# Performance work log

Measured on AMD Instinct MI355X. Metric: run time of the kernel, lower is better.

## Reference

```python
import jax, jax.numpy as jnp
import numpy as np

B, T, D = 4, 1024, 1024
H, DH = 8, 128           # heads, dim_head = dim // heads
E, FF = 8, 2048          # num_experts, expert hidden_dim
LN_EPS = 1e-5


def setup_inputs() -> dict:
    key = jax.random.key(0)
    ks = jax.random.split(key, 20)
    s = 0.02
    inp = {
        'v': jax.random.normal(ks[0], (B, T, D), jnp.float32),
        'k': jax.random.normal(ks[1], (B, T, D), jnp.float32),
        'q': jax.random.normal(ks[2], (B, T, D), jnp.float32),
        'noise': jax.random.normal(ks[3], (B * T, E), jnp.float32),
        # LayerNorm params (norm_v, norm_k, norm_q, norm_moe, moe output norm)
        'g_v': jnp.ones((D,)), 'b_v': jnp.zeros((D,)),
        'g_k': jnp.ones((D,)), 'b_k': jnp.zeros((D,)),
        'g_q': jnp.ones((D,)), 'b_q': jnp.zeros((D,)),
        'g_moe': jnp.ones((D,)), 'b_moe': jnp.zeros((D,)),
        'g_out': jnp.ones((D,)), 'b_out': jnp.zeros((D,)),
        # LinearAttention projections (q/k/v have no bias, out_proj has bias)
        'Wq': jax.random.normal(ks[4], (D, H * DH), jnp.float32) * s,
        'Wk': jax.random.normal(ks[5], (D, H * DH), jnp.float32) * s,
        'Wv': jax.random.normal(ks[6], (D, H * DH), jnp.float32) * s,
        'Wo': jax.random.normal(ks[7], (H * DH, D), jnp.float32) * s,
        'bo': jnp.zeros((D,)),
        # Router
        'Wr': jax.random.normal(ks[8], (D, E), jnp.float32) * s,
        'br': jnp.zeros((E,)),
        # Experts (stacked): dim -> FF -> dim
        'W1': jax.random.normal(ks[9], (E, D, FF), jnp.float32) * s,
        'b1': jnp.zeros((E, FF)),
        'W2': jax.random.normal(ks[10], (E, FF, D), jnp.float32) * s,
        'b2': jnp.zeros((E, D)),
        'top_k': 2,
    }
    return inp


def _ln(x, g, b):
    mu = x.mean(-1, keepdims=True)
    x0 = x - mu
    var = (x0 * x0).mean(-1, keepdims=True)
    return x0 * jax.lax.rsqrt(var + LN_EPS) * g + b


def reference(v, k, q, noise, g_v, b_v, g_k, b_k, g_q, b_q, g_moe, b_moe,
              g_out, b_out, Wq, Wk, Wv, Wo, bo, Wr, br, W1, b1, W2, b2, top_k):
    # --- LinearAttention over pre-normed v,k,q ---
    qh = jnp.einsum('btd,de->bte', _ln(q, g_q, b_q), Wq).reshape(B, T, H, DH)
    kh = jnp.einsum('btd,de->bte', _ln(k, g_k, b_k), Wk).reshape(B, T, H, DH)
    vh = jnp.einsum('btd,de->bte', _ln(v, g_v, b_v), Wv).reshape(B, T, H, DH)
    qf = jax.nn.elu(qh) + 1.0
    kf = jax.nn.elu(kh) + 1.0
    kv = jnp.einsum('bthd,bthe->bhde', kf, vh)          # [B,H,DH,DH]
    out = jnp.einsum('bthd,bhde->bthe', qf, kv)         # [B,T,H,DH]
    k_sum = kf.sum(axis=1) + 1e-6                       # [B,H,DH]
    denom = jnp.einsum('bthd,bhd->bth', qf, k_sum)[..., None]
    out = out / denom
    attn_out = jnp.einsum('bte,ed->btd', out.reshape(B, T, H * DH), Wo) + bo

    q_res = q + attn_out

    # --- MoEBlock: noisy top-k routing + expert MLPs + residual + LayerNorm ---
    x = _ln(q_res, g_moe, b_moe)
    xf = x.reshape(B * T, D)
    logits = xf @ Wr + br + noise * 0.1                 # noisy gating (randn/10)
    scores = jax.nn.softmax(logits, axis=-1)
    topk_s, topk_i = jax.lax.top_k(scores, top_k)       # [N,K]
    combine = (jax.nn.one_hot(topk_i, E, dtype=scores.dtype) * topk_s[..., None]).sum(1)  # [N,E]
    h = jax.nn.gelu(jnp.einsum('nd,edh->enh', xf, W1) + b1[:, None, :], approximate=False)
    eo = jnp.einsum('enh,ehd->end', h, W2) + b2[:, None, :]
    moe = jnp.einsum('end,ne->nd', eo, combine)         # weighted combine == masked dispatch
    moe_out = _ln(moe.reshape(B, T, D) + x, g_out, b_out)

    return q_res + moe_out
```

## Files before the change

### kernel.cpp

```cpp
#include <hip/hip_runtime.h>
#include <math.h>

typedef __attribute__((ext_vector_type(8))) short short8;
typedef __attribute__((ext_vector_type(4))) float f32x4;

#define LN_EPS 1e-5f

__device__ __forceinline__ float bf2f(unsigned short u) {
  unsigned int x = ((unsigned int)u) << 16;
  float f;
  __builtin_memcpy(&f, &x, 4);
  return f;
}
__device__ __forceinline__ unsigned short f2bf(float f) {
  unsigned int x;
  __builtin_memcpy(&x, &f, 4);
  x += 0x7fffu + ((x >> 16) & 1u);
  return (unsigned short)(x >> 16);
}

__device__ __forceinline__ void gload16(const void* g, void* l) {
  __builtin_amdgcn_global_load_lds(
      (__attribute__((address_space(1))) void*)(void*)g,
      (__attribute__((address_space(3))) void*)l, 16, 0, 0);
}

__device__ __forceinline__ void blockReduce2(float& a, float& b, float* s8) {
#pragma unroll
  for (int off = 32; off > 0; off >>= 1) {
    a += __shfl_down(a, off);
    b += __shfl_down(b, off);
  }
  const int w = threadIdx.x >> 6;
  if ((threadIdx.x & 63) == 0) { s8[w] = a; s8[4 + w] = b; }
  __syncthreads();
  a = s8[0] + s8[1] + s8[2] + s8[3];
  b = s8[4] + s8[5] + s8[6] + s8[7];
}

__global__ __launch_bounds__(256) void ln3_kernel(
    const float* __restrict__ q, const float* __restrict__ k, const float* __restrict__ v,
    const float* __restrict__ gq, const float* __restrict__ bq,
    const float* __restrict__ gk, const float* __restrict__ bk,
    const float* __restrict__ gv, const float* __restrict__ bv,
    unsigned short* __restrict__ oq, unsigned short* __restrict__ ok,
    unsigned short* __restrict__ ov) {
  __shared__ float s8[8];
  const int row = blockIdx.x, which = blockIdx.y;
  const float* x = which == 0 ? q : which == 1 ? k : v;
  const float* g = which == 0 ? gq : which == 1 ? gk : gv;
  const float* b = which == 0 ? bq : which == 1 ? bk : bv;
  unsigned short* o = which == 0 ? oq : which == 1 ? ok : ov;
  const float4 xv = ((const float4*)(x + (size_t)row * 1024))[threadIdx.x];
  float s = xv.x + xv.y + xv.z + xv.w;
  float s2 = xv.x * xv.x + xv.y * xv.y + xv.z * xv.z + xv.w * xv.w;
  blockReduce2(s, s2, s8);
  const float mu = s * (1.f / 1024.f);
  const float rs = rsqrtf(s2 * (1.f / 1024.f) - mu * mu + LN_EPS);
  const int c = threadIdx.x * 4;
  const float y[4] = {xv.x, xv.y, xv.z, xv.w};
#pragma unroll
  for (int j = 0; j < 4; ++j)
    o[(size_t)row * 1024 + c + j] = f2bf((y[j] - mu) * rs * g[c + j] + b[c + j]);
}

__global__ __launch_bounds__(256) void ln_moe_router_kernel(
    const float* __restrict__ qres, const float* __restrict__ g, const float* __restrict__ b,
    const float* __restrict__ Wr, const float* __restrict__ br,
    const float* __restrict__ noise,
    float* __restrict__ xf, unsigned short* __restrict__ xb,
    int* __restrict__ pick, float* __restrict__ pw) {
  __shared__ float s8[8];
  __shared__ float sacc[32];
  const int row = blockIdx.x;
  const float4 xv = ((const float4*)(qres + (size_t)row * 1024))[threadIdx.x];
  float s = xv.x + xv.y + xv.z + xv.w;
  float s2 = xv.x * xv.x + xv.y * xv.y + xv.z * xv.z + xv.w * xv.w;
  blockReduce2(s, s2, s8);
  const float mu = s * (1.f / 1024.f);
  const float rs = rsqrtf(s2 * (1.f / 1024.f) - mu * mu + LN_EPS);
  const int c = threadIdx.x * 4;
  const float yin[4] = {xv.x, xv.y, xv.z, xv.w};
  float y[4];
#pragma unroll
  for (int j = 0; j < 4; ++j) {
    y[j] = (yin[j] - mu) * rs * g[c + j] + b[c + j];
    xf[(size_t)row * 1024 + c + j] = y[j];
    xb[(size_t)row * 1024 + c + j] = f2bf(y[j]);
  }
  float acc[8] = {};
  const float4* wrv = (const float4*)(Wr + (size_t)c * 8);
#pragma unroll
  for (int j = 0; j < 4; ++j) {
    const float4 w0 = wrv[j * 2], w1 = wrv[j * 2 + 1];
    acc[0] += y[j] * w0.x; acc[1] += y[j] * w0.y;
    acc[2] += y[j] * w0.z; acc[3] += y[j] * w0.w;
    acc[4] += y[j] * w1.x; acc[5] += y[j] * w1.y;
    acc[6] += y[j] * w1.z; acc[7] += y[j] * w1.w;
  }
#pragma unroll
  for (int off = 32; off > 0; off >>= 1)
#pragma unroll
    for (int e = 0; e < 8; ++e) acc[e] += __shfl_down(acc[e], off);
  const int w = threadIdx.x >> 6;
  if ((threadIdx.x & 63) == 0)
#pragma unroll
    for (int e = 0; e < 8; ++e) sacc[w * 8 + e] = acc[e];
  __syncthreads();
  if (threadIdx.x == 0) {
    float lg[8], mx = -1e30f;
#pragma unroll
    for (int e = 0; e < 8; ++e) {
      lg[e] = sacc[e] + sacc[8 + e] + sacc[16 + e] + sacc[24 + e] + br[e] +
              0.1f * noise[(size_t)row * 8 + e];
      mx = fmaxf(mx, lg[e]);
    }
    float ssum = 0.f;
#pragma unroll
    for (int e = 0; e < 8; ++e) { lg[e] = expf(lg[e] - mx); ssum += lg[e]; }
    const float inv = 1.f / ssum;
#pragma unroll
    for (int e = 0; e < 8; ++e) lg[e] *= inv;
    int i1 = -1, i2 = -1;
    float m1 = -1.f, m2 = -1.f;
#pragma unroll
    for (int e = 0; e < 8; ++e) {
      if (lg[e] > m1) { m2 = m1; i2 = i1; m1 = lg[e]; i1 = e; }
      else if (lg[e] > m2) { m2 = lg[e]; i2 = e; }
    }
    pick[row * 2] = i1; pick[row * 2 + 1] = i2;
    pw[row * 2] = m1;  pw[row * 2 + 1] = m2;
  }
}

__global__ __launch_bounds__(1024) void route_build_kernel(
    const int* __restrict__ pick, const float* __restrict__ pw,
    int* __restrict__ seg, int* __restrict__ tok, float* __restrict__ wgt,
    int* __restrict__ slt) {
  __shared__ int cnt[8];
  __shared__ int segs[9];
  __shared__ int cur[8];
  const int tid = threadIdx.x;
  if (tid < 8) { cnt[tid] = 0; cur[tid] = 0; }
  __syncthreads();
  for (int i = tid; i < 8192; i += 1024) atomicAdd(&cnt[pick[i]], 1);
  __syncthreads();
  if (tid == 0) {
    int o = 0;
    for (int e = 0; e < 8; ++e) { segs[e] = o; o += (cnt[e] + 127) & ~127; }
    segs[8] = o;
  }
  __syncthreads();
  for (int i = tid; i < 9216; i += 1024) tok[i] = -1;
  if (tid < 9) seg[tid] = segs[tid];
  __syncthreads();
  for (int i = tid; i < 8192; i += 1024) {
    const int n = i >> 1, sl = i & 1;
    const int e = pick[i];
    const int p = atomicAdd(&cur[e], 1);
    const int gr = segs[e] + p;
    tok[gr] = n;
    wgt[gr] = pw[i];
    slt[gr] = sl;
  }
}

__global__ __launch_bounds__(256) void final_kernel(
    const float* __restrict__ eoS, const float* __restrict__ xf,
    const float* __restrict__ qres, const float* __restrict__ g,
    const float* __restrict__ b, float* __restrict__ out) {
  __shared__ float s8[8];
  const int row = blockIdx.x;
  const size_t SLOT = (size_t)4096 * 1024;
  const float4 m0 = ((const float4*)(eoS + (size_t)row * 1024))[threadIdx.x];
  const float4 m1 = ((const float4*)(eoS + SLOT + (size_t)row * 1024))[threadIdx.x];
  const float4 xv = ((const float4*)(xf + (size_t)row * 1024))[threadIdx.x];
  float y[4] = {m0.x + m1.x + xv.x, m0.y + m1.y + xv.y, m0.z + m1.z + xv.z,
                m0.w + m1.w + xv.w};
  float s = y[0] + y[1] + y[2] + y[3];
  float s2 = y[0] * y[0] + y[1] * y[1] + y[2] * y[2] + y[3] * y[3];
  blockReduce2(s, s2, s8);
  const float mu = s * (1.f / 1024.f);
  const float rs = rsqrtf(s2 * (1.f / 1024.f) - mu * mu + LN_EPS);
  const int c = threadIdx.x * 4;
#pragma unroll
  for (int j = 0; j < 4; ++j) {
    const size_t idx = (size_t)row * 1024 + c + j;
    out[idx] = qres[idx] + (y[j] - mu) * rs * g[c + j] + b[c + j];
  }
}

__global__ __launch_bounds__(256) void transposeB_kernel(
    const float* const* __restrict__ ins, unsigned short* const* __restrict__ outs,
    int R, int C) {
  __shared__ float t[32][33];
  const float* inz = ins[blockIdx.z];
  unsigned short* outz = outs[blockIdx.z];
  const int bx = blockIdx.x, by = blockIdx.y;
  const int tx = threadIdx.x & 31, ty = threadIdx.x >> 5;
#pragma unroll
  for (int i = 0; i < 32; i += 8)
    t[ty + i][tx] = inz[(size_t)(by * 32 + ty + i) * C + bx * 32 + tx];
  __syncthreads();
#pragma unroll
  for (int i = 0; i < 32; i += 8)
    outz[(size_t)(bx * 32 + ty + i) * R + by * 32 + tx] = f2bf(t[tx][ty + i]);
}

__global__ __launch_bounds__(256) void transpose8_kernel(
    const float* __restrict__ in, unsigned short* __restrict__ out, int R, int C) {
  __shared__ float t[32][33];
  const float* inz = in + (size_t)blockIdx.z * R * C;
  unsigned short* outz = out + (size_t)blockIdx.z * R * C;
  const int bx = blockIdx.x, by = blockIdx.y;
  const int tx = threadIdx.x & 31, ty = threadIdx.x >> 5;
#pragma unroll
  for (int i = 0; i < 32; i += 8)
    t[ty + i][tx] = inz[(size_t)(by * 32 + ty + i) * C + bx * 32 + tx];
  __syncthreads();
#pragma unroll
  for (int i = 0; i < 32; i += 8)
    outz[(size_t)(bx * 32 + ty + i) * R + by * 32 + tx] = f2bf(t[tx][ty + i]);
}

#define GEMM_BODY(GA0, GA1, GB, KDIM)                                              \
  f32x4 acc[4][4] = {};                                                            \
  for (int k0 = 0; k0 < (KDIM); k0 += 32) {                                        \
    gload16((GA0) + k0, lA);                                                       \
    gload16((GA1) + k0, lA + 16 * 32);                                             \
    gload16((GB) + k0, lB);                                                        \
    gload16((GB) + (size_t)16 * (KDIM) + k0, lB + 16 * 32);                        \
    __syncthreads();                                                               \
    short8 af[4], bfr[4];                                                          \
    const int arow = wr * 64 + (lane & 15);                                        \
    const int brow = wc * 64 + (lane & 15);                                        \
    const int kk = (lane >> 4) * 8;                                                \
    _Pragma("unroll") for (int m = 0; m < 4; ++m)                                  \
        af[m] = *(const short8*)&As[(arow + m * 16) * 32 + kk];                    \
    _Pragma("unroll") for (int n = 0; n < 4; ++n)                                  \
        bfr[n] = *(const short8*)&Bs[(brow + n * 16) * 32 + kk];                   \
    _Pragma("unroll") for (int m = 0; m < 4; ++m)                                  \
        _Pragma("unroll") for (int n = 0; n < 4; ++n)                              \
            acc[m][n] =                                                            \
                __builtin_amdgcn_mfma_f32_16x16x32_bf16(af[m], bfr[n], acc[m][n],  \
                                                        0, 0, 0);                  \
    __syncthreads();                                                               \
  }

__global__ __launch_bounds__(256) void gemm_qkv(
    const unsigned short* __restrict__ lnq, const unsigned short* __restrict__ lnk,
    const unsigned short* __restrict__ lnv, const unsigned short* __restrict__ WqT,
    const unsigned short* __restrict__ WkT, const unsigned short* __restrict__ WvT,
    unsigned short* __restrict__ qf, unsigned short* __restrict__ kf,
    unsigned short* __restrict__ vh) {
  __shared__ __align__(16) unsigned short As[128 * 32];
  __shared__ __align__(16) unsigned short Bs[128 * 32];
  const int z = blockIdx.z;
  const unsigned short* A = z == 0 ? lnq : z == 1 ? lnk : lnv;
  const unsigned short* Bt = z == 0 ? WqT : z == 1 ? WkT : WvT;
  unsigned short* outb = z == 0 ? qf : z == 1 ? kf : vh;
  const int K = 1024, N = 1024;
  const int tid = threadIdx.x;
  const int lane = tid & 63, w = tid >> 6;
  const int wr = w >> 1, wc = w & 1;
  const int row0 = blockIdx.y * 128, col0 = blockIdx.x * 128;
  const int sr = lane >> 2, sc = (lane & 3) * 8;
  const unsigned short* gA = A + (size_t)(row0 + w * 32 + sr) * K + sc;
  const unsigned short* gB = Bt + (size_t)(col0 + w * 32 + sr) * K + sc;
  unsigned short* lA = &As[(w * 32) * 32];
  unsigned short* lB = &Bs[(w * 32) * 32];
  GEMM_BODY(gA, gA + (size_t)16 * K, gB, K)
#pragma unroll
  for (int m = 0; m < 4; ++m) {
    const int rbase = row0 + wr * 64 + m * 16 + (lane >> 4) * 4;
#pragma unroll
    for (int n = 0; n < 4; ++n) {
      const int c = col0 + wc * 64 + n * 16 + (lane & 15);
#pragma unroll
      for (int r = 0; r < 4; ++r) {
        float v = acc[m][n][r];
        if (z < 2) v = v > 0.f ? v + 1.f : __expf(v);
        outb[(size_t)(rbase + r) * N + c] = f2bf(v);
      }
    }
  }
}

__global__ __launch_bounds__(256) void gemm_wo(
    const unsigned short* __restrict__ A, const unsigned short* __restrict__ Bt,
    float* __restrict__ outf, const float* __restrict__ bias,
    const float* __restrict__ addm) {
  __shared__ __align__(16) unsigned short As[128 * 32];
  __shared__ __align__(16) unsigned short Bs[128 * 32];
  const int K = 1024, N = 1024;
  const int tid = threadIdx.x;
  const int lane = tid & 63, w = tid >> 6;
  const int wr = w >> 1, wc = w & 1;
  const int row0 = blockIdx.y * 128, col0 = blockIdx.x * 128;
  const int sr = lane >> 2, sc = (lane & 3) * 8;
  const unsigned short* gA = A + (size_t)(row0 + w * 32 + sr) * K + sc;
  const unsigned short* gB = Bt + (size_t)(col0 + w * 32 + sr) * K + sc;
  unsigned short* lA = &As[(w * 32) * 32];
  unsigned short* lB = &Bs[(w * 32) * 32];
  GEMM_BODY(gA, gA + (size_t)16 * K, gB, K)
#pragma unroll
  for (int m = 0; m < 4; ++m) {
    const int rbase = row0 + wr * 64 + m * 16 + (lane >> 4) * 4;
#pragma unroll
    for (int n = 0; n < 4; ++n) {
      const int c = col0 + wc * 64 + n * 16 + (lane & 15);
#pragma unroll
      for (int r = 0; r < 4; ++r) {
        const size_t idx = (size_t)(rbase + r) * N + c;
        outf[idx] = acc[m][n][r] + bias[c] + addm[idx];
      }
    }
  }
}

template <int PHASE>
__global__ __launch_bounds__(256) void gemm_moe(
    const unsigned short* __restrict__ Asrc, const unsigned short* __restrict__ Ball,
    const float* __restrict__ bias_all, int K, int N,
    const int* __restrict__ seg, const int* __restrict__ tok,
    const float* __restrict__ wgt, const int* __restrict__ slt,
    unsigned short* __restrict__ Hb, float* __restrict__ eoS) {
  __shared__ __align__(16) unsigned short As[128 * 32];
  __shared__ __align__(16) unsigned short Bs[128 * 32];
  const int row0 = blockIdx.y * 128;
  if (row0 >= seg[8]) return;
  int e = 0;
  while (e < 7 && row0 >= seg[e + 1]) ++e;
  const int col0 = blockIdx.x * 128;
  const int tid = threadIdx.x;
  const int lane = tid & 63, w = tid >> 6;
  const int wr = w >> 1, wc = w & 1;
  const int sr = lane >> 2, sc = (lane & 3) * 8;
  const unsigned short* Bt = Ball + (size_t)e * N * K;

  const int gr0 = row0 + w * 32 + sr;
  const int gr1 = gr0 + 16;
  const unsigned short* gA0;
  const unsigned short* gA1;
  if constexpr (PHASE == 1) {
    const int t0 = tok[gr0], t1 = tok[gr1];
    gA0 = Asrc + (size_t)(t0 < 0 ? 0 : t0) * K + sc;
    gA1 = Asrc + (size_t)(t1 < 0 ? 0 : t1) * K + sc;
  } else {
    gA0 = Asrc + (size_t)gr0 * K + sc;
    gA1 = Asrc + (size_t)gr1 * K + sc;
  }
  const unsigned short* gB = Bt + (size_t)(col0 + w * 32 + sr) * K + sc;
  unsigned short* lA = &As[(w * 32) * 32];
  unsigned short* lB = &Bs[(w * 32) * 32];
  GEMM_BODY(gA0, gA1, gB, K)
#pragma unroll
  for (int m = 0; m < 4; ++m) {
    const int rloc = wr * 64 + m * 16 + (lane >> 4) * 4;
#pragma unroll
    for (int n = 0; n < 4; ++n) {
      const int c = col0 + wc * 64 + n * 16 + (lane & 15);
#pragma unroll
      for (int r = 0; r < 4; ++r) {
        const int gr = row0 + rloc + r;
        float v = acc[m][n][r] + bias_all[(size_t)e * N + c];
        if constexpr (PHASE == 1) {
          v = 0.5f * v * (1.f + erff(v * 0.70710678118654752f));
          Hb[(size_t)gr * N + c] = f2bf(v);
        } else {
          const int t = tok[gr];
          if (t >= 0)
            eoS[(size_t)slt[gr] * (4096 * 1024) + (size_t)t * N + c] = wgt[gr] * v;
        }
      }
    }
  }
}

__global__ __launch_bounds__(256) void kvpart_kernel(
    const unsigned short* __restrict__ kf, const unsigned short* __restrict__ vh,
    float* __restrict__ kvp, float* __restrict__ ksp) {
  const int bh = blockIdx.x;
  const int b = bh >> 3, h = bh & 7;
  const int ch = blockIdx.y;
  const int tid = threadIdx.x;
  const int d0 = (tid >> 4) * 8, e0 = (tid & 15) * 8;
  __shared__ unsigned short kb[64][128];
  __shared__ unsigned short vb[64][128];
  for (int i = tid; i < 1024; i += 256) {
    const int tt = i >> 4, dd = (i & 15) * 8;
    const size_t base = ((size_t)((b * 1024 + ch * 64 + tt) * 8 + h)) * 128 + dd;
    *(short8*)&kb[tt][dd] = *(const short8*)&kf[base];
    *(short8*)&vb[tt][dd] = *(const short8*)&vh[base];
  }
  __syncthreads();
  float acc[8][8] = {};
  float ks[8] = {};
  for (int tt = 0; tt < 64; ++tt) {
    float kv8[8], vv8[8];
    const short8 kr = *(const short8*)&kb[tt][d0];
    const short8 vr = *(const short8*)&vb[tt][e0];
#pragma unroll
    for (int j = 0; j < 8; ++j) {
      kv8[j] = bf2f((unsigned short)kr[j]);
      vv8[j] = bf2f((unsigned short)vr[j]);
    }
#pragma unroll
    for (int i = 0; i < 8; ++i)
#pragma unroll
      for (int j = 0; j < 8; ++j) acc[i][j] += kv8[i] * vv8[j];
    if ((tid & 15) == 0)
#pragma unroll
      for (int i = 0; i < 8; ++i) ks[i] += kv8[i];
  }
  const size_t obase = ((size_t)(ch * 32 + bh) * 128) * 128;
#pragma unroll
  for (int i = 0; i < 8; ++i)
#pragma unroll
    for (int j = 0; j < 8; ++j)
      kvp[obase + (size_t)(d0 + i) * 128 + e0 + j] = acc[i][j];
  if ((tid & 15) == 0)
#pragma unroll
    for (int i = 0; i < 8; ++i) ksp[(size_t)(ch * 32 + bh) * 128 + d0 + i] = ks[i];
}

__global__ __launch_bounds__(256) void kvreduce_kernel(
    const float* __restrict__ kvp, const float* __restrict__ ksp,
    unsigned short* __restrict__ kvb, float* __restrict__ ksum) {
  const int idx = blockIdx.x * 256 + threadIdx.x;
  const int CS = 32 * 128 * 128;
  float s = 0.f;
#pragma unroll
  for (int c = 0; c < 16; ++c) s += kvp[(size_t)c * CS + idx];
  kvb[idx] = f2bf(s);
  if (idx < 32 * 128) {
    float t = 1e-6f;
#pragma unroll
    for (int c = 0; c < 16; ++c) t += ksp[c * 4096 + idx];
    ksum[idx] = t;
  }
}

__global__ __launch_bounds__(256) void attnout_kernel(
    const unsigned short* __restrict__ qf, const unsigned short* __restrict__ kvb,
    const float* __restrict__ ksum, unsigned short* __restrict__ ctx) {
  const int bh = blockIdx.x, b = bh >> 3, h = bh & 7;
  const int tb = blockIdx.y;
  const int tid = threadIdx.x;
  __shared__ unsigned short kvl[128 * 128];
  __shared__ float ksl[128];
  __shared__ float denom[128];
  __shared__ unsigned short qfl[128 * 32];
  for (int i = tid; i < 16384; i += 256) kvl[i] = kvb[(size_t)bh * 16384 + i];
  if (tid < 128) ksl[tid] = ksum[bh * 128 + tid];
  __syncthreads();
  if (tid < 128) {
    const int t = tb * 128 + tid;
    const size_t qbase = ((size_t)((b * 1024 + t) * 8 + h)) * 128;
    float s = 0.f;
    for (int d = 0; d < 128; ++d) s += bf2f(qf[qbase + d]) * ksl[d];
    denom[tid] = s;
  }
  float acc[8][8] = {};
  const int t0 = (tid >> 4) * 8, e0 = (tid & 15) * 8;
  for (int dc = 0; dc < 128; dc += 32) {
    __syncthreads();
    for (int i = tid; i < 128 * 32; i += 256) {
      const int tt = i >> 5, dd = i & 31;
      qfl[i] = qf[((size_t)((b * 1024 + tb * 128 + tt) * 8 + h)) * 128 + dc + dd];
    }
    __syncthreads();
    for (int dd = 0; dd < 32; ++dd) {
      float kvrow[8];
#pragma unroll
      for (int j = 0; j < 8; ++j) kvrow[j] = bf2f(kvl[(dc + dd) * 128 + e0 + j]);
#pragma unroll
      for (int i = 0; i < 8; ++i) {
        const float qv = bf2f(qfl[(t0 + i) * 32 + dd]);
#pragma unroll
        for (int j = 0; j < 8; ++j) acc[i][j] += qv * kvrow[j];
      }
    }
  }
  __syncthreads();
#pragma unroll
  for (int i = 0; i < 8; ++i) {
    const int t = tb * 128 + t0 + i;
    const float inv = 1.f / denom[t0 + i];
#pragma unroll
    for (int j = 0; j < 8; ++j)
      ctx[((size_t)(b * 1024 + t)) * 1024 + h * 128 + e0 + j] = f2bf(acc[i][j] * inv);
  }
}

__global__ void setptr_kernel(const float* Wq, const float* Wk, const float* Wv,
                              const float* Wo, unsigned short* WqT, unsigned short* WkT,
                              unsigned short* WvT, unsigned short* WoT,
                              const float** ins, unsigned short** outs) {
  if (threadIdx.x == 0) {
    ins[0] = Wq; ins[1] = Wk; ins[2] = Wv; ins[3] = Wo;
    outs[0] = WqT; outs[1] = WkT; outs[2] = WvT; outs[3] = WoT;
  }
}

extern "C" void kernel_launch(void* const* d_in, const int* in_sizes, int n_in,
                              void* d_out, int out_size, void* d_ws, size_t ws_size,
                              hipStream_t stream) {
  (void)in_sizes; (void)n_in; (void)out_size; (void)ws_size;
  const float* vin  = (const float*)d_in[0];
  const float* kin  = (const float*)d_in[1];
  const float* qin  = (const float*)d_in[2];
  const float* noise = (const float*)d_in[3];
  const float* g_v = (const float*)d_in[4];  const float* b_v = (const float*)d_in[5];
  const float* g_k = (const float*)d_in[6];  const float* b_k = (const float*)d_in[7];
  const float* g_q = (const float*)d_in[8];  const float* b_q = (const float*)d_in[9];
  const float* g_moe = (const float*)d_in[10]; const float* b_moe = (const float*)d_in[11];
  const float* g_out = (const float*)d_in[12]; const float* b_out = (const float*)d_in[13];
  const float* Wq = (const float*)d_in[14];
  const float* Wk = (const float*)d_in[15];
  const float* Wv = (const float*)d_in[16];
  const float* Wo = (const float*)d_in[17];
  const float* bo = (const float*)d_in[18];
  const float* Wr = (const float*)d_in[19];
  const float* br = (const float*)d_in[20];
  const float* W1 = (const float*)d_in[21];
  const float* b1 = (const float*)d_in[22];
  const float* W2 = (const float*)d_in[23];
  const float* b2 = (const float*)d_in[24];
  float* out = (float*)d_out;

  const int NT = 4096, D = 1024, FF = 2048;
  const int MAXR = 9216;

  char* p = (char*)d_ws;
  auto alloc = [&](size_t bytes) {
    void* r = (void*)p;
    p += (bytes + 255) & ~(size_t)255;
    return r;
  };
  char* base0 = p;
  unsigned short* lnq = (unsigned short*)alloc((size_t)NT * D * 2);
  unsigned short* lnk = (unsigned short*)alloc((size_t)NT * D * 2);
  unsigned short* lnv = (unsigned short*)alloc((size_t)NT * D * 2);
  unsigned short* WqT = (unsigned short*)alloc((size_t)D * D * 2);
  unsigned short* WkT = (unsigned short*)alloc((size_t)D * D * 2);
  unsigned short* WvT = (unsigned short*)alloc((size_t)D * D * 2);
  unsigned short* WoT = (unsigned short*)alloc((size_t)D * D * 2);
  unsigned short* qf  = (unsigned short*)alloc((size_t)NT * D * 2);
  unsigned short* kf  = (unsigned short*)alloc((size_t)NT * D * 2);
  unsigned short* vh  = (unsigned short*)alloc((size_t)NT * D * 2);
  unsigned short* kvb = (unsigned short*)alloc((size_t)32 * 128 * 128 * 2);
  float* ksp  = (float*)alloc((size_t)16 * 32 * 128 * 4);
  float* ksum = (float*)alloc((size_t)32 * 128 * 4);
  unsigned short* ctx = (unsigned short*)alloc((size_t)NT * D * 2);
  float* qres = (float*)alloc((size_t)NT * D * 4);
  float* xf   = (float*)alloc((size_t)NT * D * 4);
  unsigned short* xb = (unsigned short*)alloc((size_t)NT * D * 2);
  unsigned short* W1T_all = (unsigned short*)alloc((size_t)8 * D * FF * 2);
  unsigned short* W2T_all = (unsigned short*)alloc((size_t)8 * FF * D * 2);
  float* eoS = (float*)alloc((size_t)2 * NT * D * 4);
  int* pick = (int*)alloc((size_t)NT * 2 * 4);
  float* pw = (float*)alloc((size_t)NT * 2 * 4);
  int* seg = (int*)alloc(9 * 4);
  int* tokl = (int*)alloc(MAXR * 4);
  float* wgt = (float*)alloc(MAXR * 4);
  int* slt = (int*)alloc(MAXR * 4);
  const float** tins = (const float**)alloc(4 * sizeof(void*));
  unsigned short** touts = (unsigned short**)alloc(4 * sizeof(void*));
  float* kvp = eoS;
  unsigned short* Hb = (unsigned short*)base0;

  setptr_kernel<<<dim3(1), 64, 0, stream>>>(Wq, Wk, Wv, Wo, WqT, WkT, WvT, WoT,
                                            tins, touts);
  transposeB_kernel<<<dim3(32, 32, 4), 256, 0, stream>>>(tins, touts, D, D);

  ln3_kernel<<<dim3(NT, 3), 256, 0, stream>>>(qin, kin, vin, g_q, b_q, g_k, b_k, g_v, b_v,
                                              lnq, lnk, lnv);

  gemm_qkv<<<dim3(D / 128, NT / 128, 3), 256, 0, stream>>>(lnq, lnk, lnv, WqT, WkT, WvT,
                                                           qf, kf, vh);

  kvpart_kernel<<<dim3(32, 16), 256, 0, stream>>>(kf, vh, kvp, ksp);
  kvreduce_kernel<<<dim3(2048), 256, 0, stream>>>(kvp, ksp, kvb, ksum);
  attnout_kernel<<<dim3(32, 8), 256, 0, stream>>>(qf, kvb, ksum, ctx);

  gemm_wo<<<dim3(D / 128, NT / 128), 256, 0, stream>>>(ctx, WoT, qres, bo, qin);

  ln_moe_router_kernel<<<dim3(NT), 256, 0, stream>>>(qres, g_moe, b_moe, Wr, br, noise,
                                                     xf, xb, pick, pw);
  route_build_kernel<<<dim3(1), 1024, 0, stream>>>(pick, pw, seg, tokl, wgt, slt);

  transpose8_kernel<<<dim3(FF / 32, D / 32, 8), 256, 0, stream>>>(W1, W1T_all, D, FF);
  transpose8_kernel<<<dim3(D / 32, FF / 32, 8), 256, 0, stream>>>(W2, W2T_all, FF, D);

  gemm_moe<1><<<dim3(FF / 128, MAXR / 128), 256, 0, stream>>>(
      xb, W1T_all, b1, D, FF, seg, tokl, wgt, slt, Hb, nullptr);
  gemm_moe<2><<<dim3(D / 128, MAXR / 128), 256, 0, stream>>>(
      Hb, W2T_all, b2, FF, D, seg, tokl, wgt, slt, nullptr, eoS);

  final_kernel<<<dim3(NT), 256, 0, stream>>>(eoS, xf, qres, g_out, b_out, out);
}
```

Measured before the change: 424.5 us.

## Double-buffer GEMM LDS tiles, add XCD block swizzle, specialize MoE K

Rewrites the shared GEMM main loop to use two LDS buffers, so the global-to-LDS load of the next K slice is issued while MFMAs run on the current one. It also remaps workgroup IDs so neighbouring tiles land on the same XCD for better L2 reuse, and makes the MoE GEMM K dimension a compile-time constant. This doubles LDS use per block, which may lower occupancy, and the swizzle assumes the tile count divides evenly by 8.

```diff
diff --git a/kernel.cpp b/kernel.cpp
--- a/kernel.cpp
+++ b/kernel.cpp
@@ -23,6 +23,16 @@
   __builtin_amdgcn_global_load_lds(
       (__attribute__((address_space(1))) void*)(void*)g,
       (__attribute__((address_space(3))) void*)l, 16, 0, 0);
+}
+
+__device__ __forceinline__ void xcd_swizzle(int& bx, int& by) {
+  const int nx = gridDim.x;
+  const int nwg = nx * gridDim.y;
+  const int orig = blockIdx.y * nx + blockIdx.x;
+  const int cpx = nwg >> 3;
+  const int lid = (orig & 7) * cpx + (orig >> 3);
+  bx = lid % nx;
+  by = lid / nx;
 }
 
 __device__ __forceinline__ void blockReduce2(float& a, float& b, float* s8) {
@@ -223,29 +233,51 @@
     outz[(size_t)(bx * 32 + ty + i) * R + by * 32 + tx] = f2bf(t[tx][ty + i]);
 }
 
-#define GEMM_BODY(GA0, GA1, GB, KDIM)                                              \
-  f32x4 acc[4][4] = {};                                                            \
-  for (int k0 = 0; k0 < (KDIM); k0 += 32) {                                        \
-    gload16((GA0) + k0, lA);                                                       \
-    gload16((GA1) + k0, lA + 16 * 32);                                             \
-    gload16((GB) + k0, lB);                                                        \
-    gload16((GB) + (size_t)16 * (KDIM) + k0, lB + 16 * 32);                        \
-    __syncthreads();                                                               \
-    short8 af[4], bfr[4];                                                          \
-    const int arow = wr * 64 + (lane & 15);                                        \
-    const int brow = wc * 64 + (lane & 15);                                        \
-    const int kk = (lane >> 4) * 8;                                                \
-    _Pragma("unroll") for (int m = 0; m < 4; ++m)                                  \
-        af[m] = *(const short8*)&As[(arow + m * 16) * 32 + kk];                    \
-    _Pragma("unroll") for (int n = 0; n < 4; ++n)                                  \
-        bfr[n] = *(const short8*)&Bs[(brow + n * 16) * 32 + kk];                   \
-    _Pragma("unroll") for (int m = 0; m < 4; ++m)                                  \
-        _Pragma("unroll") for (int n = 0; n < 4; ++n)                              \
-            acc[m][n] =                                                            \
-                __builtin_amdgcn_mfma_f32_16x16x32_bf16(af[m], bfr[n], acc[m][n],  \
-                                                        0, 0, 0);                  \
-    __syncthreads();                                                               \
-  }
+#define GEMM_STAGE(buf, k0, KD)                                              \
+  gload16(gA0 + (k0), lA + (buf) * 4096);                                    \
+  gload16(gA1 + (k0), lA + (buf) * 4096 + 16 * 32);                          \
+  gload16(gB + (k0), lB + (buf) * 4096);                                     \
+  gload16(gB + (size_t)16 * (KD) + (k0), lB + (buf) * 4096 + 16 * 32);
+
+#define GEMM_COMPUTE(buf)                                                    \
+  {                                                                          \
+    const unsigned short* sA = &As[buf][0];                                  \
+    const unsigned short* sB = &Bs[buf][0];                                  \
+    short8 af[4], bfr[4];                                                    \
+    _Pragma("unroll") for (int m = 0; m < 4; ++m)                            \
+        af[m] = *(const short8*)&sA[(arow + m * 16) * 32 + kk];              \
+    _Pragma("unroll") for (int n = 0; n < 4; ++n)                            \
+        bfr[n] = *(const short8*)&sB[(brow + n * 16) * 32 + kk];             \
+    _Pragma("unroll") for (int m = 0; m < 4; ++m)                            \
+      _Pragma("unroll") for (int n = 0; n < 4; ++n)                          \
+        acc[m][n] = __builtin_amdgcn_mfma_f32_16x16x32_bf16(                 \
+            af[m], bfr[n], acc[m][n], 0, 0, 0);                              \
+  }
+
+#define GEMM_LOOP(KD)                                                        \
+  GEMM_STAGE(0, 0, KD)                                                       \
+  __syncthreads();                                                           \
+  for (int k0 = 0; k0 < (KD); k0 += 64) {                                    \
+    GEMM_STAGE(1, k0 + 32, KD)                                               \
+    GEMM_COMPUTE(0)                                                          \
+    __syncthreads();                                                         \
+    if (k0 + 64 < (KD)) { GEMM_STAGE(0, k0 + 64, KD) }                       \
+    GEMM_COMPUTE(1)                                                          \
+    __syncthreads();                                                         \
+  }
+
+#define GEMM_PREAMBLE                                                        \
+  __shared__ __align__(16) unsigned short As[2][128 * 32];                   \
+  __shared__ __align__(16) unsigned short Bs[2][128 * 32];                   \
+  const int tid = threadIdx.x;                                               \
+  const int lane = tid & 63, w = tid >> 6;                                   \
+  const int wr = w >> 1, wc = w & 1;                                         \
+  const int sr = lane >> 2, sc = (lane & 3) * 8;                             \
+  const int arow = wr * 64 + (lane & 15);                                    \
+  const int brow = wc * 64 + (lane & 15);                                    \
+  const int kk = (lane >> 4) * 8;                                            \
+  unsigned short* lA = &As[0][(w * 32) * 32];                                \
+  unsigned short* lB = &Bs[0][(w * 32) * 32];
 
 __global__ __launch_bounds__(256) void gemm_qkv(
     const unsigned short* __restrict__ lnq, const unsigned short* __restrict__ lnk,
@@ -253,23 +285,20 @@
     const unsigned short* __restrict__ WkT, const unsigned short* __restrict__ WvT,
     unsigned short* __restrict__ qf, unsigned short* __restrict__ kf,
     unsigned short* __restrict__ vh) {
-  __shared__ __align__(16) unsigned short As[128 * 32];
-  __shared__ __align__(16) unsigned short Bs[128 * 32];
   const int z = blockIdx.z;
   const unsigned short* A = z == 0 ? lnq : z == 1 ? lnk : lnv;
   const unsigned short* Bt = z == 0 ? WqT : z == 1 ? WkT : WvT;
   unsigned short* outb = z == 0 ? qf : z == 1 ? kf : vh;
   const int K = 1024, N = 1024;
-  const int tid = threadIdx.x;
-  const int lane = tid & 63, w = tid >> 6;
-  const int wr = w >> 1, wc = w & 1;
-  const int row0 = blockIdx.y * 128, col0 = blockIdx.x * 128;
-  const int sr = lane >> 2, sc = (lane & 3) * 8;
-  const unsigned short* gA = A + (size_t)(row0 + w * 32 + sr) * K + sc;
+  GEMM_PREAMBLE
+  int bx, by;
+  xcd_swizzle(bx, by);
+  const int row0 = by * 128, col0 = bx * 128;
+  const unsigned short* gA0 = A + (size_t)(row0 + w * 32 + sr) * K + sc;
+  const unsigned short* gA1 = gA0 + (size_t)16 * K;
   const unsigned short* gB = Bt + (size_t)(col0 + w * 32 + sr) * K + sc;
-  unsigned short* lA = &As[(w * 32) * 32];
-  unsigned short* lB = &Bs[(w * 32) * 32];
-  GEMM_BODY(gA, gA + (size_t)16 * K, gB, K)
+  f32x4 acc[4][4] = {};
+  GEMM_LOOP(1024)
 #pragma unroll
   for (int m = 0; m < 4; ++m) {
     const int rbase = row0 + wr * 64 + m * 16 + (lane >> 4) * 4;
@@ -290,19 +319,16 @@
     const unsigned short* __restrict__ A, const unsigned short* __restrict__ Bt,
     float* __restrict__ outf, const float* __restrict__ bias,
     const float* __restrict__ addm) {
-  __shared__ __align__(16) unsigned short As[128 * 32];
-  __shared__ __align__(16) unsigned short Bs[128 * 32];
   const int K = 1024, N = 1024;
-  const int tid = threadIdx.x;
-  const int lane = tid & 63, w = tid >> 6;
-  const int wr = w >> 1, wc = w & 1;
-  const int row0 = blockIdx.y * 128, col0 = blockIdx.x * 128;
-  const int sr = lane >> 2, sc = (lane & 3) * 8;
-  const unsigned short* gA = A + (size_t)(row0 + w * 32 + sr) * K + sc;
+  GEMM_PREAMBLE
+  int bx, by;
+  xcd_swizzle(bx, by);
+  const int row0 = by * 128, col0 = bx * 128;
+  const unsigned short* gA0 = A + (size_t)(row0 + w * 32 + sr) * K + sc;
+  const unsigned short* gA1 = gA0 + (size_t)16 * K;
   const unsigned short* gB = Bt + (size_t)(col0 + w * 32 + sr) * K + sc;
-  unsigned short* lA = &As[(w * 32) * 32];
-  unsigned short* lB = &Bs[(w * 32) * 32];
-  GEMM_BODY(gA, gA + (size_t)16 * K, gB, K)
+  f32x4 acc[4][4] = {};
+  GEMM_LOOP(1024)
 #pragma unroll
   for (int m = 0; m < 4; ++m) {
     const int rbase = row0 + wr * 64 + m * 16 + (lane >> 4) * 4;
@@ -321,23 +347,20 @@
 template <int PHASE>
 __global__ __launch_bounds__(256) void gemm_moe(
     const unsigned short* __restrict__ Asrc, const unsigned short* __restrict__ Ball,
-    const float* __restrict__ bias_all, int K, int N,
+    const float* __restrict__ bias_all, int Kdim, int N,
     const int* __restrict__ seg, const int* __restrict__ tok,
     const float* __restrict__ wgt, const int* __restrict__ slt,
     unsigned short* __restrict__ Hb, float* __restrict__ eoS) {
-  __shared__ __align__(16) unsigned short As[128 * 32];
-  __shared__ __align__(16) unsigned short Bs[128 * 32];
-  const int row0 = blockIdx.y * 128;
+  const int K = PHASE == 1 ? 1024 : 2048;
+  GEMM_PREAMBLE
+  int bx, by;
+  xcd_swizzle(bx, by);
+  const int row0 = by * 128;
   if (row0 >= seg[8]) return;
   int e = 0;
   while (e < 7 && row0 >= seg[e + 1]) ++e;
-  const int col0 = blockIdx.x * 128;
-  const int tid = threadIdx.x;
-  const int lane = tid & 63, w = tid >> 6;
-  const int wr = w >> 1, wc = w & 1;
-  const int sr = lane >> 2, sc = (lane & 3) * 8;
+  const int col0 = bx * 128;
   const unsigned short* Bt = Ball + (size_t)e * N * K;
-
   const int gr0 = row0 + w * 32 + sr;
   const int gr1 = gr0 + 16;
   const unsigned short* gA0;
@@ -351,9 +374,9 @@
     gA1 = Asrc + (size_t)gr1 * K + sc;
   }
   const unsigned short* gB = Bt + (size_t)(col0 + w * 32 + sr) * K + sc;
-  unsigned short* lA = &As[(w * 32) * 32];
-  unsigned short* lB = &Bs[(w * 32) * 32];
-  GEMM_BODY(gA0, gA1, gB, K)
+  f32x4 acc[4][4] = {};
+  if constexpr (PHASE == 1) { GEMM_LOOP(1024) }
+  else { GEMM_LOOP(2048) }
 #pragma unroll
   for (int m = 0; m < 4; ++m) {
     const int rloc = wr * 64 + m * 16 + (lane >> 4) * 4;
@@ -594,9 +617,9 @@
   transpose8_kernel<<<dim3(D / 32, FF / 32, 8), 256, 0, stream>>>(W2, W2T_all, FF, D);
 
   gemm_moe<1><<<dim3(FF / 128, MAXR / 128), 256, 0, stream>>>(
-      xb, W1T_all, b1, D, FF, seg, tokl, wgt, slt, Hb, nullptr);
+      xb, W1T_all, b1, 1024, FF, seg, tokl, wgt, slt, Hb, nullptr);
   gemm_moe<2><<<dim3(D / 128, MAXR / 128), 256, 0, stream>>>(
-      Hb, W2T_all, b2, FF, D, seg, tokl, wgt, slt, nullptr, eoS);
+      Hb, W2T_all, b2, 2048, D, seg, tokl, wgt, slt, nullptr, eoS);
 
   final_kernel<<<dim3(NT), 256, 0, stream>>>(eoS, xf, qres, g_out, b_out, out);
 }
```

Measured after the change: 388.8 us. 1.09x faster.
